# Optimization experiments

Measured on AMD Instinct MI355X. Metric: run time of the kernel, lower is better.

## Reference

```python
import jax, jax.numpy as jnp
import numpy as np

T = 8           # number of merged tables
N = 100000      # rows per table
D = 128         # embedding_dim
B = 16384       # bags (batch) per table
L = 20          # multi-hot bag size -> total indices per table
TOTAL = B * L


def setup_inputs() -> dict:
    key = jax.random.key(0)
    kw, ki = jax.random.split(key)
    weights = jax.random.normal(kw, (T, N, D), dtype=jnp.float32) * 0.01
    indices = jax.random.randint(ki, (T, TOTAL), 0, N, dtype=jnp.int64 if jax.config.jax_enable_x64 else jnp.int32)
    # offsets: start position of each bag; fixed-size bags of length L (include_last_offset=False)
    offsets = jnp.broadcast_to(jnp.arange(B, dtype=indices.dtype) * L, (T, B))
    return {"weights": weights, "indices": indices, "offsets": offsets}


def reference(weights, indices, offsets):
    """Merged EmbeddingBag forward, pooling_mode='sum', include_last_offset=False.

    weights: [T, N, D] float; indices: [T, total] int; offsets: [T, B] int.
    Returns [T, B, D] (stack of the per-table (B, D) outputs).
    """
    total = indices.shape[1]
    nbags = offsets.shape[1]

    def one_table(w, idx, off):
        # bag id of each index: last offset <= position (EmbeddingBag semantics)
        pos = jnp.arange(total)
        seg = jnp.searchsorted(off, pos, side="right") - 1  # [total]
        rows = w[idx]  # gather: [total, D]
        return jax.ops.segment_sum(rows, seg, num_segments=nbags)  # [B, D]

    return jax.vmap(one_table)(weights, indices, offsets)
```

## Files before the change

kernel.cpp:

```cpp
#include <hip/hip_runtime.h>

#define T_TABLES 8
#define N_ROWS   100000
#define DIM      128
#define BAGS     16384
#define BAG_L    20
#define TOTAL_IDX (BAGS * BAG_L)

#define DV (DIM / 4)

__global__ __launch_bounds__(256) void merged_embbag_kernel(
    const float4* __restrict__ weights,
    const int*    __restrict__ indices,
    const int*    __restrict__ offsets,
    float4*       __restrict__ out)
{
    int gid = blockIdx.x * blockDim.x + threadIdx.x;
    int c  = gid & (DV - 1);
    int tb = gid >> 5;
    int b  = tb & (BAGS - 1);
    int t  = tb >> 14;

    const int* off = offsets + t * BAGS;
    int start = off[b];
    int end   = (b == BAGS - 1) ? TOTAL_IDX : off[b + 1];
    int n = end - start;

    const int*    idx = indices + (size_t)t * TOTAL_IDX + start;
    const float4* w   = weights + (size_t)t * N_ROWS * DV + c;

    float4 acc = make_float4(0.f, 0.f, 0.f, 0.f);

    if (n == BAG_L) {
        int rows[BAG_L];
        #pragma unroll
        for (int j = 0; j < BAG_L; ++j) rows[j] = idx[j];

        float4 v[BAG_L];
        #pragma unroll
        for (int j = 0; j < BAG_L; ++j) v[j] = w[(size_t)rows[j] * DV];

        #pragma unroll
        for (int j = 0; j < BAG_L; ++j) {
            acc.x += v[j].x; acc.y += v[j].y; acc.z += v[j].z; acc.w += v[j].w;
        }
    } else {
        for (int p = 0; p < n; ++p) {
            int row = idx[p];
            float4 v = w[(size_t)row * DV];
            acc.x += v.x; acc.y += v.y; acc.z += v.z; acc.w += v.w;
        }
    }

    out[gid] = acc;
}

extern "C" void kernel_launch(void* const* d_in, const int* in_sizes, int n_in,
                              void* d_out, int out_size, void* d_ws, size_t ws_size,
                              hipStream_t stream) {
    const float4* weights = (const float4*)d_in[0];
    const int*    indices = (const int*)d_in[1];
    const int*    offsets = (const int*)d_in[2];
    float4*       out     = (float4*)d_out;

    const int total_threads = T_TABLES * BAGS * DV;
    const int block = 256;
    const int grid  = (total_threads + block - 1) / block;
    merged_embbag_kernel<<<grid, block, 0, stream>>>(weights, indices, offsets, out);
}
```

Before: 612.3 us.

## Map one wavefront per bag with float2 lanes and scalarized indices

Reassigns work so that each 64-lane wavefront handles one bag, with every lane loading a float2 slice of the 128-wide row instead of 32 threads each loading a float4. Offsets and indices are made wave-uniform with readfirstlane so they can be handled as scalar values, and the output is written with nontemporal stores. The goal is to cut redundant per-lane index loads and to use full wavefronts per row gather. In exchange, each load is narrower, so more memory instructions are issued per row.

```diff
diff --git a/kernel.cpp b/kernel.cpp
--- a/kernel.cpp
+++ b/kernel.cpp
@@ -7,64 +7,70 @@
 #define BAG_L    20
 #define TOTAL_IDX (BAGS * BAG_L)
 
-#define DV (DIM / 4)
+#define DV2 (DIM / 2)
+
+typedef float v2f __attribute__((ext_vector_type(2)));
 
 __global__ __launch_bounds__(256) void merged_embbag_kernel(
-    const float4* __restrict__ weights,
+    const float2* __restrict__ weights,
     const int*    __restrict__ indices,
     const int*    __restrict__ offsets,
-    float4*       __restrict__ out)
+    float2*       __restrict__ out)
 {
-    int gid = blockIdx.x * blockDim.x + threadIdx.x;
-    int c  = gid & (DV - 1);
-    int tb = gid >> 5;
-    int b  = tb & (BAGS - 1);
-    int t  = tb >> 14;
+    const int lane = threadIdx.x & 63;
+
+    const int wid = __builtin_amdgcn_readfirstlane(
+        (int)(blockIdx.x * 4 + (threadIdx.x >> 6)));
+    const int b = wid & (BAGS - 1);
+    const int t = wid >> 14;
 
     const int* off = offsets + t * BAGS;
-    int start = off[b];
-    int end   = (b == BAGS - 1) ? TOTAL_IDX : off[b + 1];
-    int n = end - start;
+    const int start = __builtin_amdgcn_readfirstlane(off[b]);
+    const int end   = (b == BAGS - 1)
+                        ? TOTAL_IDX
+                        : __builtin_amdgcn_readfirstlane(off[b + 1]);
+    const int n = end - start;
 
-    const int*    idx = indices + (size_t)t * TOTAL_IDX + start;
-    const float4* w   = weights + (size_t)t * N_ROWS * DV + c;
+    const int*    idx   = indices + (size_t)t * TOTAL_IDX + start;
+    const float2* wbase = weights + (size_t)t * N_ROWS * DV2;
 
-    float4 acc = make_float4(0.f, 0.f, 0.f, 0.f);
+    float2 acc = make_float2(0.f, 0.f);
 
-    if (n == BAG_L) {
+    if (__builtin_expect(n == BAG_L, 1)) {
         int rows[BAG_L];
         #pragma unroll
-        for (int j = 0; j < BAG_L; ++j) rows[j] = idx[j];
+        for (int j = 0; j < BAG_L; ++j)
+            rows[j] = __builtin_amdgcn_readfirstlane(idx[j]);
 
-        float4 v[BAG_L];
+        float2 v[BAG_L];
         #pragma unroll
-        for (int j = 0; j < BAG_L; ++j) v[j] = w[(size_t)rows[j] * DV];
+        for (int j = 0; j < BAG_L; ++j)
+            v[j] = wbase[(size_t)rows[j] * DV2 + lane];
 
         #pragma unroll
-        for (int j = 0; j < BAG_L; ++j) {
-            acc.x += v[j].x; acc.y += v[j].y; acc.z += v[j].z; acc.w += v[j].w;
-        }
+        for (int j = 0; j < BAG_L; ++j) { acc.x += v[j].x; acc.y += v[j].y; }
     } else {
         for (int p = 0; p < n; ++p) {
-            int row = idx[p];
-            float4 v = w[(size_t)row * DV];
-            acc.x += v.x; acc.y += v.y; acc.z += v.z; acc.w += v.w;
+            int row = __builtin_amdgcn_readfirstlane(idx[p]);
+            float2 v = wbase[(size_t)row * DV2 + lane];
+            acc.x += v.x; acc.y += v.y;
         }
     }
 
-    out[gid] = acc;
+    v2f val; val.x = acc.x; val.y = acc.y;
+    __builtin_nontemporal_store(val, (v2f*)(out + (size_t)wid * DV2 + lane));
 }
 
 extern "C" void kernel_launch(void* const* d_in, const int* in_sizes, int n_in,
                               void* d_out, int out_size, void* d_ws, size_t ws_size,
                               hipStream_t stream) {
-    const float4* weights = (const float4*)d_in[0];
+    const float2* weights = (const float2*)d_in[0];
     const int*    indices = (const int*)d_in[1];
     const int*    offsets = (const int*)d_in[2];
-    float4*       out     = (float4*)d_out;
+    float2*       out     = (float2*)d_out;
 
-    const int total_threads = T_TABLES * BAGS * DV;
+    const int total_waves = T_TABLES * BAGS;
     const int block = 256;
-    const int grid  = (total_threads + block - 1) / block;
+    const int grid  = total_waves / 4;
     merged_embbag_kernel<<<grid, block, 0, stream>>>(weights, indices, offsets, out);
 }
```

After: 614.2 us. No clear change (+0.3%).
